# Kernel optimization log

Measured on AMD Instinct MI355X. Metric: run time of the kernel, lower is better.

The kernel has to match this reference:

```python
import jax, jax.numpy as jnp
import numpy as np

H, W = 1024, 2048
K_CENTERS = 32          # fixed-size stand-in for torch.nonzero(center_heatmap > 0)
ROAD_ID = 0             # cityscapes trainId for 'road'
THING_START = 11        # cityscapes thing classes are trainIds >= 11
LABEL_DIVISOR = 1000
FILTER_IDS = (10, 19)   # 'sky', 'ego vehicle' depth filter classes
EPS = 1e-8


def _group_instances(heat, off, sem):
    # heat: (H,W) f32, off: (2,H,W) f32 [dy,dx], sem: (1,H,W) int
    vals, idx = jax.lax.top_k(heat.reshape(-1), K_CENTERS)
    cy = (idx // W).astype(jnp.float32)
    cx = (idx % W).astype(jnp.float32)
    valid = vals > 0.0
    ys = jnp.arange(H, dtype=jnp.float32)[:, None] + off[0]   # (H,W)
    xs = jnp.arange(W, dtype=jnp.float32)[None, :] + off[1]   # (H,W)
    d2 = (ys[None] - cy[:, None, None]) ** 2 + (xs[None] - cx[:, None, None]) ** 2  # (K,H,W)
    d2 = jnp.where(valid[:, None, None], d2, jnp.inf)
    inst = (jnp.argmin(d2, axis=0) + 1).astype(sem.dtype)     # (H,W), 1-based instance ids
    thing = sem >= THING_START
    any_valid = jnp.any(valid)
    return jnp.where(thing & any_valid, sem * LABEL_DIVISOR + inst[None], sem)


def _surface_normal(p):
    # p: (1,3,H,W) camera-space points; central-difference cross-product stencil
    px = jnp.pad(p, ((0, 0), (0, 0), (0, 0), (1, 1)), mode='edge')
    py = jnp.pad(p, ((0, 0), (0, 0), (1, 1), (0, 0)), mode='edge')
    vx = px[:, :, :, 2:] - px[:, :, :, :-2]
    vy = py[:, :, 2:, :] - py[:, :, :-2, :]
    n = jnp.cross(vx, vy, axis=1)
    return n / (jnp.linalg.norm(n, axis=1, keepdims=True) + EPS)


def setup_inputs() -> dict:
    key = jax.random.key(0)
    k1, k2, k3, k4 = jax.random.split(key, 4)
    sem_seg = jax.random.randint(k1, (1, 1, H, W), 0, 19, dtype=jnp.int64)
    center_heatmap = jax.random.normal(k2, (1, 1, H, W), dtype=jnp.float32) - 3.0
    offsets = jax.random.normal(k3, (1, 2, H, W), dtype=jnp.float32) * 5.0
    depth_logits = jax.random.uniform(k4, (1, 1, H, W), dtype=jnp.float32, minval=0.5, maxval=80.0)
    K_mat = np.array([[2262.52, 0.0, 1096.98], [0.0, 2265.30, 513.14], [0.0, 0.0, 1.0]], dtype=np.float32)
    inverse_camera_matrix = jnp.asarray(np.linalg.inv(K_mat), dtype=jnp.float32)
    real_camera_height = jnp.ones((1,), dtype=jnp.float32) * 1.7
    return {"sem_seg": sem_seg, "center_heatmap": center_heatmap, "offsets": offsets,
            "depth_logits": depth_logits, "inverse_camera_matrix": inverse_camera_matrix,
            "real_camera_height": real_camera_height}


def reference(sem_seg, center_heatmap, offsets, depth_logits, inverse_camera_matrix, real_camera_height):
    sem = sem_seg[0]                       # (1,H,W) int
    sem = _group_instances(center_heatmap[0, 0], offsets[0], sem)
    # pixel grid -> normalized camera rays
    xm = jnp.broadcast_to(jnp.arange(W, dtype=jnp.float32)[None, :], (H, W))
    ym = jnp.broadcast_to(jnp.arange(H, dtype=jnp.float32)[:, None], (H, W))
    grid = jnp.stack([xm, ym, jnp.ones((H, W), jnp.float32)], axis=0)           # (3,H,W)
    xnorm = jnp.einsum('ij,jhw->ihw', inverse_camera_matrix, grid)[None]        # (1,3,H,W)
    cam_points = xnorm * depth_logits                                           # (1,3,H,W)
    ground = sem == ROAD_ID                                                     # (1,H,W)
    normal = _surface_normal(cam_points)
    cam_heights = jnp.abs(jnp.sum(cam_points * normal, axis=1))                 # (1,H,W)
    # masked lower-median (torch.median semantics): sort with inf padding
    vals = jnp.where(ground, cam_heights, jnp.inf).reshape(-1)
    cnt = jnp.sum(ground.astype(jnp.int32))
    med_idx = jnp.maximum((cnt - 1) // 2, 0)
    cam_height = jnp.sort(vals)[med_idx]
    scale = real_camera_height.reshape(()) / cam_height
    depth = depth_logits * scale
    cam_points = cam_points * scale
    filt = (sem == FILTER_IDS[0])
    for cid in FILTER_IDS[1:]:
        filt = filt | (sem == cid)
    depth = jnp.where(filt[:, None], 0.0, depth)                                # (1,1,H,W)
    cam_out = jnp.concatenate([cam_points[0], sem.astype(jnp.float32)], axis=0).transpose(1, 2, 0)  # (H,W,4)
    return sem.astype(jnp.int32), depth[0], cam_out
```

## Files before the change

### kernel.cpp

```cpp
#include <hip/hip_runtime.h>
#include <math.h>

#define HH 1024
#define WW 2048
#define HW (HH*WW)
#define KC 32
#define NW 8192
#define CREGW 8
#define KCAP 12288
#define NMED 128
#define SENT 0xFFFFFFFFu
#define BIAS 16777216.0f

typedef unsigned long long u64;

struct Scratch {
  unsigned hist0[2048];
  unsigned hist1[2048];
  unsigned hist2[2048];
  unsigned done0;
  int nvalid;
  float scale;
  float ck[KC], m2cy[KC], m2cx[KC];
  unsigned ccnt[NW];
  unsigned cblk[NW];
};

__device__ __forceinline__ unsigned agent_load(const unsigned* p){
  return __hip_atomic_load(p, __ATOMIC_RELAXED, __HIP_MEMORY_SCOPE_AGENT);
}

template<int CTRL>
__device__ __forceinline__ u64 dpp_mov64(u64 x){
  unsigned lo = (unsigned)x, hi = (unsigned)(x>>32);
  unsigned nlo = (unsigned)__builtin_amdgcn_update_dpp((int)lo, (int)lo, CTRL, 0xF, 0xF, false);
  unsigned nhi = (unsigned)__builtin_amdgcn_update_dpp((int)hi, (int)hi, CTRL, 0xF, 0xF, false);
  return ((u64)nhi<<32) | (u64)nlo;
}
__device__ __forceinline__ u64 wave_max64(u64 x){
  u64 y;
  y = dpp_mov64<0x111>(x); if (y > x) x = y;
  y = dpp_mov64<0x112>(x); if (y > x) x = y;
  y = dpp_mov64<0x114>(x); if (y > x) x = y;
  y = dpp_mov64<0x118>(x); if (y > x) x = y;
  y = dpp_mov64<0x142>(x); if (y > x) x = y;
  y = dpp_mov64<0x143>(x); if (y > x) x = y;
  unsigned mlo = (unsigned)__builtin_amdgcn_readlane((int)(unsigned)x, 63);
  unsigned mhi = (unsigned)__builtin_amdgcn_readlane((int)(unsigned)(x>>32), 63);
  return ((u64)mhi<<32) | (u64)mlo;
}

#define CSWAP(a,b) { if ((b) > (a)) { u64 _t=(a); (a)=(b); (b)=_t; } }

__device__ __forceinline__ void grid_bar(unsigned* ctr, unsigned target){
  __syncthreads();
  if (threadIdx.x == 0){
    atomicAdd(ctr, 1u);
    while (__hip_atomic_load(ctr, __ATOMIC_RELAXED, __HIP_MEMORY_SCOPE_AGENT) < target)
      __builtin_amdgcn_s_sleep(2);
  }
  __syncthreads();
}

template<int PASS>
__device__ __forceinline__ void pick512(const unsigned* gh, unsigned* wsumL, unsigned* res){
  int t = threadIdx.x;
  unsigned v0 = agent_load(&gh[t*4+0]);
  unsigned v1 = agent_load(&gh[t*4+1]);
  unsigned v2 = agent_load(&gh[t*4+2]);
  unsigned v3 = agent_load(&gh[t*4+3]);
  int kin_prev = (PASS==0) ? 0 : (int)res[1];
  unsigned s = v0+v1+v2+v3;
  unsigned incl = s;
  #pragma unroll
  for (int d=1; d<64; d<<=1){ unsigned o = __shfl_up(incl, d); if ((t&63) >= d) incl += o; }
  unsigned excl = incl - s;
  if ((t&63)==63) wsumL[t>>6] = incl;
  __syncthreads();
  unsigned woff=0, total=0;
  #pragma unroll
  for (int w=0;w<8;w++){ unsigned xw=wsumL[w]; if (w < (t>>6)) woff += xw; total += xw; }
  unsigned pre = woff + excl;
  int k = (PASS==0) ? ((total>0) ? (int)((total-1)>>1) : 0) : kin_prev;
  if (total>0 && (unsigned)k >= pre && (unsigned)k < pre + s){
    unsigned kr = (unsigned)k - pre;
    int b_ = t*4;
    if (kr >= v0){ kr -= v0; b_++;
      if (kr >= v1){ kr -= v1; b_++;
        if (kr >= v2){ kr -= v2; b_++; } } }
    res[0] = (unsigned)b_; res[1] = kr;
  }
  if (t==0) res[2] = total;
  __syncthreads();
}

__global__ __launch_bounds__(256) void kA(const float* __restrict__ heat,
    const int* __restrict__ sem, const float* __restrict__ depth,
    const float* __restrict__ invK, u64* __restrict__ cand,
    unsigned* __restrict__ cheight, Scratch* __restrict__ sc){
  int t = threadIdx.x;
  if (blockIdx.x == 0){
    unsigned* hz = sc->hist0;
    for (int j=t; j<6144; j+=256) hz[j] = 0u;
    if (t==0) sc->done0 = 0u;
  }
  int i4 = blockIdx.x*256 + t;
  int p = i4<<2;
  int y = p>>11, x = p&2047;
  int row = y<<11;
  int lane = t & 63;
  unsigned wid = (unsigned)(blockIdx.x*4 + (t>>6));

  float4 hq = ((const float4*)heat)[i4];
  int4   s4 = ((const int4*)sem)[i4];
  float4 dc = ((const float4*)depth)[i4];
  float  dl = depth[row + (x>0 ? x-1 : 0)];
  float  dr = depth[row + (x+4<WW ? x+4 : WW-1)];
  int rowu = (y>0)?    row-WW : row;
  int rowd = (y<HH-1)? row+WW : row;
  float4 du = ((const float4*)(depth + rowu))[x>>2];
  float4 dd = ((const float4*)(depth + rowd))[x>>2];
  float ik0=invK[0],ik1=invK[1],ik2=invK[2];
  float ik3=invK[3],ik4=invK[4],ik5=invK[5];
  float ik6=invK[6],ik7=invK[7],ik8=invK[8];

  float hv[4] = {hq.x,hq.y,hq.z,hq.w};
  int   sv[4] = {s4.x,s4.y,s4.z,s4.w};
  float dcv[4]= {dc.x,dc.y,dc.z,dc.w};
  float duv[4]= {du.x,du.y,du.z,du.w};
  float ddv[4]= {dd.x,dd.y,dd.z,dd.w};

  unsigned npos = 0, ng = 0;
  #pragma unroll
  for (int j=0;j<4;j++){ npos += (hv[j] > 0.0f) ? 1u : 0u; ng += (sv[j]==0) ? 1u : 0u; }
  unsigned incc = npos, incg = ng;
  #pragma unroll
  for (int d=1; d<64; d<<=1){
    unsigned oc = __shfl_up(incc, d), og = __shfl_up(incg, d);
    if (lane >= d){ incc += oc; incg += og; }
  }

  float fy = (float)y;
  float a0=ik1*fy+ik2, a1=ik4*fy+ik5, a2=ik7*fy+ik8;
  float fyu=(y>0)?    fy-1.0f : fy;
  float fyd=(y<HH-1)? fy+1.0f : fy;
  float uu0=ik1*fyu+ik2, uu1=ik4*fyu+ik5, uu2=ik7*fyu+ik8;
  float ww0=ik1*fyd+ik2, ww1=ik4*fyd+ik5, ww2=ik7*fyd+ik8;
  float dxmv[4] = {dl, dcv[0], dcv[1], dcv[2]};
  float dxpv[4] = {dcv[1], dcv[2], dcv[3], dr};
  float h[4];
  #pragma unroll
  for (int j=0;j<4;j++){
    float fx  = (float)(x+j);
    float fxm = (x+j>0)?    fx-1.0f : fx;
    float fxp = (x+j<WW-1)? fx+1.0f : fx;
    float pc0=(ik0*fx +a0)*dcv[j],  pc1=(ik3*fx +a1)*dcv[j],  pc2=(ik6*fx +a2)*dcv[j];
    float pm0=(ik0*fxm+a0)*dxmv[j], pm1=(ik3*fxm+a1)*dxmv[j], pm2=(ik6*fxm+a2)*dxmv[j];
    float pp0=(ik0*fxp+a0)*dxpv[j], pp1=(ik3*fxp+a1)*dxpv[j], pp2=(ik6*fxp+a2)*dxpv[j];
    float pu0=(ik0*fx+uu0)*duv[j],  pu1=(ik3*fx+uu1)*duv[j],  pu2=(ik6*fx+uu2)*duv[j];
    float pd0=(ik0*fx+ww0)*ddv[j],  pd1=(ik3*fx+ww1)*ddv[j],  pd2=(ik6*fx+ww2)*ddv[j];
    float vx0=pp0-pm0, vx1=pp1-pm1, vx2=pp2-pm2;
    float vy0=pd0-pu0, vy1=pd1-pu1, vy2=pd2-pu2;
    float n0=vx1*vy2-vx2*vy1, n1=vx2*vy0-vx0*vy2, n2=vx0*vy1-vx1*vy0;
    float nn = sqrtf(n0*n0+n1*n1+n2*n2) + 1e-8f;
    h[j] = fabsf(pc0*n0+pc1*n1+pc2*n2) / nn;
  }

  if (npos){
    unsigned cslot = incc - npos;
    u64* cb = cand + ((size_t)wid * CREGW);
    #pragma unroll
    for (int j=0;j<4;j++){
      if (hv[j] > 0.0f){
        if (cslot < CREGW)
          cb[cslot] = ((u64)__float_as_uint(hv[j])<<32) | (u64)(unsigned)(~(unsigned)(p+j));
        cslot++;
      }
    }
  }
  if (ng){
    unsigned gslot = (wid<<8) + (incg - ng);
    #pragma unroll
    for (int j=0;j<4;j++){
      if (sv[j]==0){ cheight[gslot++] = __float_as_uint(h[j]); }
    }
  }
  if (lane == 63){
    sc->ccnt[wid] = (incc > CREGW) ? CREGW : incc;
    sc->cblk[wid] = incg;
  }
}

__global__ __launch_bounds__(64) void k_top(const u64* __restrict__ cand,
    const Scratch* __restrict__ sc, u64* __restrict__ tour){
  __shared__ unsigned cnt32[32];
  int lane = threadIdx.x;
  int b = blockIdx.x, r0 = b*32;
  if (lane < 32) cnt32[lane] = sc->ccnt[r0+lane];
  __syncthreads();
  int s0 = lane*4;
  u64 t0 = ((s0&7)     < cnt32[s0>>3])     ? cand[(size_t)r0*CREGW + s0]   : 0ULL;
  u64 t1 = (((s0+1)&7) < cnt32[(s0+1)>>3]) ? cand[(size_t)r0*CREGW + s0+1] : 0ULL;
  u64 t2 = (((s0+2)&7) < cnt32[(s0+2)>>3]) ? cand[(size_t)r0*CREGW + s0+2] : 0ULL;
  u64 t3 = (((s0+3)&7) < cnt32[(s0+3)>>3]) ? cand[(size_t)r0*CREGW + s0+3] : 0ULL;
  if (__ballot((t0|t1|t2|t3) != 0ULL) == 0ULL){
    if (lane < 32) tour[b*32 + lane] = 0ULL;
    return;
  }
  CSWAP(t0,t1) CSWAP(t2,t3) CSWAP(t0,t2) CSWAP(t1,t3) CSWAP(t1,t2)
  for (int r=0;r<32;r++){
    u64 m = wave_max64(t0);
    if (lane==0) tour[b*32+r] = m;
    if (m && t0==m){ t0=t1; t1=t2; t2=t3; t3=0ULL; }
  }
}

__global__ __launch_bounds__(512) void k_med(const unsigned* __restrict__ ch,
    const u64* __restrict__ tour, Scratch* __restrict__ sc,
    const float* __restrict__ rch){
  __shared__ unsigned keys[KCAP];
  __shared__ unsigned hsh[2048];
  __shared__ unsigned cnts[64], rstart[64];
  __shared__ unsigned wsumL[8];
  __shared__ unsigned res[3];
  __shared__ unsigned misc[2];
  __shared__ u64 mls[4*KC];
  int t = threadIdx.x;
  int b = blockIdx.x;
  int lane = t & 63;
  int w = t >> 6;

  if (b == NMED){
    const u64* lp = tour + (size_t)(w*64+lane)*KC;
    if (w < 4){
      u64 h0=lp[0], h1=lp[1], h2=lp[2], h3=lp[3];
      int pp = 0;
      for (int r=0;r<KC;r++){
        u64 m = wave_max64(h0);
        if (lane==0) mls[w*KC+r] = m;
        if (m && h0==m){ pp++; h0=h1; h1=h2; h2=h3; h3 = (pp+3<KC)? lp[pp+3] : 0ULL; }
      }
    }
    __syncthreads();
    if (w == 0){
      u64 key = (lane<4) ? mls[lane*KC] : 0ULL;
      int p2=0, kk=0;
      for (int r=0;r<KC;r++){
        u64 m = wave_max64(key);
        if (m){
          if (lane==0){
            unsigned idx = ~(unsigned)(m & 0xFFFFFFFFULL);
            float cy = (float)(idx >> 11), cx = (float)(idx & 2047u);
            sc->ck[r]   = cy*cy + cx*cx + BIAS;
            sc->m2cy[r] = -2.0f*cy;
            sc->m2cx[r] = -2.0f*cx;
          }
          if (key==m){ p2++; key = (p2<KC)? mls[lane*KC+p2] : 0ULL; }
          kk = r+1;
        }
      }
      if (lane==0) sc->nvalid = kk;
    }
    return;
  }

  int r0 = b * 64;
  if (t==0){ res[0]=0u; res[1]=0u; res[2]=0u; misc[1]=0u; }
  __syncthreads();
  if (t < 64){
    unsigned c = sc->cblk[r0 + t];
    cnts[t] = c;
    unsigned inc = c;
    #pragma unroll
    for (int d=1; d<64; d<<=1){ unsigned o = __shfl_up(inc, d); if (lane >= d) inc += o; }
    rstart[t] = (inc <= KCAP) ? (inc - c) : SENT;
    if (inc <= KCAP) atomicMax(&misc[1], inc);
    if (t == 63) misc[0] = inc;
  }
  for (int j=t;j<2048;j+=512) hsh[j]=0u;
  __syncthreads();
  unsigned total = misc[0];
  bool anyov = (total > KCAP);
  unsigned nl = anyov ? misc[1] : total;

  #pragma unroll
  for (int k=0;k<8;k++){
    int r = w + (k<<3);
    unsigned c = cnts[r], rs = rstart[r];
    if (rs != SENT){
      const unsigned* base = ch + ((size_t)(r0+r)<<8);
      for (unsigned i=lane; i<c; i+=64) keys[rs+i] = base[i];
    }
  }
  __syncthreads();

  for (unsigned i=t; i<nl; i+=512) atomicAdd(&hsh[keys[i]>>21], 1u);
  if (anyov){
    for (int r=0;r<64;r++){
      if (rstart[r]==SENT){
        unsigned c = cnts[r];
        const unsigned* base = ch + ((size_t)(r0+r)<<8);
        for (unsigned i=t;i<c;i+=512) atomicAdd(&hsh[base[i]>>21], 1u);
      }
    }
  }
  __syncthreads();
  for (int j=t;j<2048;j+=512){ unsigned v=hsh[j]; if (v) atomicAdd(&sc->hist0[j], v); }
  grid_bar(&sc->done0, NMED);
  pick512<0>(sc->hist0, wsumL, res);
  unsigned tot0 = res[2];
  unsigned pref0 = res[0];
  for (int j=t;j<2048;j+=512) hsh[j]=0u;
  __syncthreads();

  for (unsigned i=t; i<nl; i+=512){
    unsigned key = keys[i];
    if ((key>>21) == pref0) atomicAdd(&hsh[(key>>10)&2047u], 1u);
  }
  if (anyov){
    for (int r=0;r<64;r++){
      if (rstart[r]==SENT){
        unsigned c = cnts[r];
        const unsigned* base = ch + ((size_t)(r0+r)<<8);
        for (unsigned i=t;i<c;i+=512){ unsigned key=base[i]; if ((key>>21)==pref0) atomicAdd(&hsh[(key>>10)&2047u], 1u); }
      }
    }
  }
  __syncthreads();
  for (int j=t;j<2048;j+=512){ unsigned v=hsh[j]; if (v) atomicAdd(&sc->hist1[j], v); }
  grid_bar(&sc->done0, 2*NMED);
  pick512<1>(sc->hist1, wsumL, res);
  unsigned pref01 = (pref0 << 11) | res[0];
  for (int j=t;j<2048;j+=512) hsh[j]=0u;
  __syncthreads();

  for (unsigned i=t; i<nl; i+=512){
    unsigned key = keys[i];
    if ((key>>10) == pref01) atomicAdd(&hsh[key & 1023u], 1u);
  }
  if (anyov){
    for (int r=0;r<64;r++){
      if (rstart[r]==SENT){
        unsigned c = cnts[r];
        const unsigned* base = ch + ((size_t)(r0+r)<<8);
        for (unsigned i=t;i<c;i+=512){ unsigned key=base[i]; if ((key>>10)==pref01) atomicAdd(&hsh[key & 1023u], 1u); }
      }
    }
  }
  __syncthreads();
  for (int j=t;j<2048;j+=512){ unsigned v=hsh[j]; if (v) atomicAdd(&sc->hist2[j], v); }
  grid_bar(&sc->done0, 3*NMED);
  pick512<2>(sc->hist2, wsumL, res);
  if (b == 0 && t == 0){
    unsigned key = (pref01 << 10) | res[0];
    sc->scale = (tot0 > 0) ? (rch[0] / __uint_as_float(key)) : 0.0f;
  }
}

__global__ __launch_bounds__(256) void k_final(const int* __restrict__ sem,
    const float* __restrict__ off, const float* __restrict__ depth,
    const float* __restrict__ invK, const Scratch* __restrict__ sc,
    float* __restrict__ out){
  __shared__ float sck[KC], smy[KC], smx[KC];
  __shared__ int snv; __shared__ float ssc;
  int t = threadIdx.x;
  if (t < KC){ sck[t]=sc->ck[t]; smy[t]=sc->m2cy[t]; smx[t]=sc->m2cx[t]; }
  if (t == 0){ snv = sc->nvalid; ssc = sc->scale; }
  __syncthreads();

  int i4 = blockIdx.x*256 + t;
  int p = i4<<2;
  int y = p>>11, x = p&2047;
  int4   s4 = ((const int4*)sem)[i4];
  float4 oy = ((const float4*)off)[i4];
  float4 ox = ((const float4*)(off+HW))[i4];
  float4 dc = ((const float4*)depth)[i4];

  float ik0=invK[0],ik1=invK[1],ik2=invK[2];
  float ik3=invK[3],ik4=invK[4],ik5=invK[5];
  float ik6=invK[6],ik7=invK[7],ik8=invK[8];
  float fy = (float)y;
  float a0=ik1*fy+ik2, a1=ik4*fy+ik5, a2=ik7*fy+ik8;
  int nv = snv; float s = ssc;

  int   sv[4]  = {s4.x,s4.y,s4.z,s4.w};
  float oyv[4] = {oy.x,oy.y,oy.z,oy.w};
  float oxv[4] = {ox.x,ox.y,ox.z,ox.w};
  float dv[4]  = {dc.x,dc.y,dc.z,dc.w};

  float ys[4], xs[4]; unsigned ub[4];
  #pragma unroll
  for (int j=0;j<4;j++){
    ys[j] = fy + oyv[j]; xs[j] = (float)(x+j) + oxv[j]; ub[j] = SENT;
  }
  for (int k=0;k<nv;k++){
    float ckk=sck[k], my=smy[k], mx=smx[k];
    #pragma unroll
    for (int j=0;j<4;j++){
      float tt = fmaf(ys[j], my, ckk);
      tt = fmaf(xs[j], mx, tt);
      unsigned uu = (__float_as_uint(tt) & ~31u) | (unsigned)k;
      ub[j] = uu < ub[j] ? uu : ub[j];
    }
  }
  float lab[4], depo[4];
  float4* cam = (float4*)(out + (size_t)2*HW);
  #pragma unroll
  for (int j=0;j<4;j++){
    int sj = sv[j];
    lab[j] = (sj >= 11 && nv > 0) ? (float)(sj*1000 + (int)(ub[j]&31u) + 1) : (float)sj;
    float fx = (float)(x+j);
    float ds = dv[j]*s;
    float p0=(ik0*fx+a0)*ds, p1=(ik3*fx+a1)*ds, p2=(ik6*fx+a2)*ds;
    bool filt = (lab[j]==10.0f) || (lab[j]==19.0f);
    depo[j] = filt ? 0.0f : ds;
    cam[p+j] = make_float4(p0, p1, p2, lab[j]);
  }
  ((float4*)out)[i4]      = make_float4(lab[0], lab[1], lab[2], lab[3]);
  ((float4*)(out+HW))[i4] = make_float4(depo[0], depo[1], depo[2], depo[3]);
}

extern "C" void kernel_launch(void* const* d_in, const int* in_sizes, int n_in,
                              void* d_out, int out_size, void* d_ws, size_t ws_size,
                              hipStream_t stream){
  const int*   sem   = (const int*)d_in[0];
  const float* heat  = (const float*)d_in[1];
  const float* off   = (const float*)d_in[2];
  const float* depth = (const float*)d_in[3];
  const float* invK  = (const float*)d_in[4];
  const float* rch   = (const float*)d_in[5];
  float* out = (float*)d_out;

  unsigned* cheight = (unsigned*)d_ws;
  u64* cand = (u64*)((char*)d_ws + (size_t)NW*256*4);
  u64* tour = (u64*)((char*)d_ws + (size_t)NW*256*4 + (size_t)NW*CREGW*8);
  Scratch* sc = (Scratch*)((char*)d_ws + (size_t)NW*256*4 + (size_t)NW*CREGW*8 + (size_t)256*KC*8);

  const int grid4 = HW/4/256;

  kA<<<grid4, 256, 0, stream>>>(heat, sem, depth, invK, cand, cheight, sc);
  k_top<<<256, 64, 0, stream>>>(cand, sc, tour);
  k_med<<<NMED+1, 512, 0, stream>>>(cheight, tour, sc, rch);
  k_final<<<grid4, 256, 0, stream>>>(sem, off, depth, invK, sc, out);
}
```

Before: 59.40 us.

## Move first median histogram pass into k_top to drop a grid barrier

The first radix-histogram pass over the ground-height keys moves from k_med into k_top. k_top now runs 256 threads per block, and its extra waves build the top-11-bit histogram alongside the top-k tournament. k_med then reads the finished hist0 straight away, fuses the key staging into LDS with the second-level histogram, and drops one of its three grid-wide barriers. This trades a spin barrier plus one pass over the keys for a larger k_top block that reads all the height keys from global memory.

```diff
diff --git a/kernel.cpp b/kernel.cpp
--- a/kernel.cpp
+++ b/kernel.cpp
@@ -191,28 +191,45 @@
   }
 }
 
-__global__ __launch_bounds__(64) void k_top(const u64* __restrict__ cand,
-    const Scratch* __restrict__ sc, u64* __restrict__ tour){
+__global__ __launch_bounds__(256) void k_top(const u64* __restrict__ cand,
+    const unsigned* __restrict__ ch, Scratch* __restrict__ sc,
+    u64* __restrict__ tour){
   __shared__ unsigned cnt32[32];
-  int lane = threadIdx.x;
+  __shared__ unsigned gcnt[32];
+  __shared__ unsigned hsh[2048];
+  int t = threadIdx.x;
   int b = blockIdx.x, r0 = b*32;
-  if (lane < 32) cnt32[lane] = sc->ccnt[r0+lane];
-  __syncthreads();
-  int s0 = lane*4;
-  u64 t0 = ((s0&7)     < cnt32[s0>>3])     ? cand[(size_t)r0*CREGW + s0]   : 0ULL;
-  u64 t1 = (((s0+1)&7) < cnt32[(s0+1)>>3]) ? cand[(size_t)r0*CREGW + s0+1] : 0ULL;
-  u64 t2 = (((s0+2)&7) < cnt32[(s0+2)>>3]) ? cand[(size_t)r0*CREGW + s0+2] : 0ULL;
-  u64 t3 = (((s0+3)&7) < cnt32[(s0+3)>>3]) ? cand[(size_t)r0*CREGW + s0+3] : 0ULL;
-  if (__ballot((t0|t1|t2|t3) != 0ULL) == 0ULL){
-    if (lane < 32) tour[b*32 + lane] = 0ULL;
-    return;
-  }
-  CSWAP(t0,t1) CSWAP(t2,t3) CSWAP(t0,t2) CSWAP(t1,t3) CSWAP(t1,t2)
+  if (t < 32){ cnt32[t] = sc->ccnt[r0+t]; gcnt[t] = sc->cblk[r0+t]; }
+  for (int j=t;j<2048;j+=256) hsh[j]=0u;
+  __syncthreads();
+
+  if (t < 64){
+    int lane = t;
+    int s0 = lane*4;
+    u64 t0 = ((s0&7)     < cnt32[s0>>3])     ? cand[(size_t)r0*CREGW + s0]   : 0ULL;
+    u64 t1 = (((s0+1)&7) < cnt32[(s0+1)>>3]) ? cand[(size_t)r0*CREGW + s0+1] : 0ULL;
+    u64 t2 = (((s0+2)&7) < cnt32[(s0+2)>>3]) ? cand[(size_t)r0*CREGW + s0+2] : 0ULL;
+    u64 t3 = (((s0+3)&7) < cnt32[(s0+3)>>3]) ? cand[(size_t)r0*CREGW + s0+3] : 0ULL;
+    if (__ballot((t0|t1|t2|t3) != 0ULL) == 0ULL){
+      if (lane < 32) tour[b*32 + lane] = 0ULL;
+    } else {
+      CSWAP(t0,t1) CSWAP(t2,t3) CSWAP(t0,t2) CSWAP(t1,t3) CSWAP(t1,t2)
+      for (int r=0;r<32;r++){
+        u64 m = wave_max64(t0);
+        if (lane==0) tour[b*32+r] = m;
+        if (m && t0==m){ t0=t1; t1=t2; t2=t3; t3=0ULL; }
+      }
+    }
+  }
+
+  #pragma unroll 4
   for (int r=0;r<32;r++){
-    u64 m = wave_max64(t0);
-    if (lane==0) tour[b*32+r] = m;
-    if (m && t0==m){ t0=t1; t1=t2; t2=t3; t3=0ULL; }
-  }
+    unsigned c = gcnt[r];
+    const unsigned* base = ch + ((size_t)(r0+r)<<8);
+    for (unsigned i=t; i<c; i+=256) atomicAdd(&hsh[base[i]>>21], 1u);
+  }
+  __syncthreads();
+  for (int j=t;j<2048;j+=256){ unsigned v=hsh[j]; if (v) atomicAdd(&sc->hist0[j], v); }
 }
 
 __global__ __launch_bounds__(512) void k_med(const unsigned* __restrict__ ch,
@@ -283,55 +300,33 @@
   bool anyov = (total > KCAP);
   unsigned nl = anyov ? misc[1] : total;
 
+  pick512<0>(sc->hist0, wsumL, res);
+  unsigned tot0 = res[2];
+  unsigned pref0 = res[0];
+
   #pragma unroll
   for (int k=0;k<8;k++){
     int r = w + (k<<3);
     unsigned c = cnts[r], rs = rstart[r];
+    const unsigned* base = ch + ((size_t)(r0+r)<<8);
     if (rs != SENT){
-      const unsigned* base = ch + ((size_t)(r0+r)<<8);
-      for (unsigned i=lane; i<c; i+=64) keys[rs+i] = base[i];
-    }
-  }
-  __syncthreads();
-
-  for (unsigned i=t; i<nl; i+=512) atomicAdd(&hsh[keys[i]>>21], 1u);
-  if (anyov){
-    for (int r=0;r<64;r++){
-      if (rstart[r]==SENT){
-        unsigned c = cnts[r];
-        const unsigned* base = ch + ((size_t)(r0+r)<<8);
-        for (unsigned i=t;i<c;i+=512) atomicAdd(&hsh[base[i]>>21], 1u);
-      }
-    }
-  }
-  __syncthreads();
-  for (int j=t;j<2048;j+=512){ unsigned v=hsh[j]; if (v) atomicAdd(&sc->hist0[j], v); }
+      for (unsigned i=lane; i<c; i+=64){
+        unsigned key = base[i];
+        keys[rs+i] = key;
+        if ((key>>21) == pref0) atomicAdd(&hsh[(key>>10)&2047u], 1u);
+      }
+    } else {
+      for (unsigned i=lane; i<c; i+=64){
+        unsigned key = base[i];
+        if ((key>>21) == pref0) atomicAdd(&hsh[(key>>10)&2047u], 1u);
+      }
+    }
+  }
+  __syncthreads();
+  for (int j=t;j<2048;j+=512){ unsigned v=hsh[j]; if (v) atomicAdd(&sc->hist1[j], v); hsh[j]=0u; }
   grid_bar(&sc->done0, NMED);
-  pick512<0>(sc->hist0, wsumL, res);
-  unsigned tot0 = res[2];
-  unsigned pref0 = res[0];
-  for (int j=t;j<2048;j+=512) hsh[j]=0u;
-  __syncthreads();
-
-  for (unsigned i=t; i<nl; i+=512){
-    unsigned key = keys[i];
-    if ((key>>21) == pref0) atomicAdd(&hsh[(key>>10)&2047u], 1u);
-  }
-  if (anyov){
-    for (int r=0;r<64;r++){
-      if (rstart[r]==SENT){
-        unsigned c = cnts[r];
-        const unsigned* base = ch + ((size_t)(r0+r)<<8);
-        for (unsigned i=t;i<c;i+=512){ unsigned key=base[i]; if ((key>>21)==pref0) atomicAdd(&hsh[(key>>10)&2047u], 1u); }
-      }
-    }
-  }
-  __syncthreads();
-  for (int j=t;j<2048;j+=512){ unsigned v=hsh[j]; if (v) atomicAdd(&sc->hist1[j], v); }
-  grid_bar(&sc->done0, 2*NMED);
   pick512<1>(sc->hist1, wsumL, res);
   unsigned pref01 = (pref0 << 11) | res[0];
-  for (int j=t;j<2048;j+=512) hsh[j]=0u;
   __syncthreads();
 
   for (unsigned i=t; i<nl; i+=512){
@@ -349,7 +344,7 @@
   }
   __syncthreads();
   for (int j=t;j<2048;j+=512){ unsigned v=hsh[j]; if (v) atomicAdd(&sc->hist2[j], v); }
-  grid_bar(&sc->done0, 3*NMED);
+  grid_bar(&sc->done0, 2*NMED);
   pick512<2>(sc->hist2, wsumL, res);
   if (b == 0 && t == 0){
     unsigned key = (pref01 << 10) | res[0];
@@ -439,7 +434,7 @@
   const int grid4 = HW/4/256;
 
   kA<<<grid4, 256, 0, stream>>>(heat, sem, depth, invK, cand, cheight, sc);
-  k_top<<<256, 64, 0, stream>>>(cand, sc, tour);
+  k_top<<<256, 256, 0, stream>>>(cand, cheight, sc, tour);
   k_med<<<NMED+1, 512, 0, stream>>>(cheight, tour, sc, rch);
   k_final<<<grid4, 256, 0, stream>>>(sem, off, depth, invK, sc, out);
 }
```

Result: slower. 70.90 us (+19.3%).
